# Kernel tuning notes

Measured on AMD Instinct MI355X. Metric: run time of the kernel, lower is better.

The kernel has to match this reference:

```python
import jax, jax.numpy as jnp
import numpy as np

N, R, H, L, E = 50000, 16, 32, 8, 1600000


def setup_inputs() -> dict:
    key = jax.random.key(0)
    ks = jax.random.split(key, 8)
    edge_index = jax.random.randint(ks[0], (2, E), 0, N, dtype=jnp.int32)
    edge_type = jax.random.randint(ks[1], (E,), 0, R, dtype=jnp.int32)
    W1 = jax.random.normal(ks[2], (R, N, H), jnp.float32) * 0.02
    root1 = jax.random.normal(ks[3], (N, H), jnp.float32) * 0.02
    b1 = jnp.zeros((H,), jnp.float32)
    W2 = jax.random.normal(ks[4], (R, H, L), jnp.float32) * 0.1
    root2 = jax.random.normal(ks[5], (H, L), jnp.float32) * 0.1
    b2 = jnp.zeros((L,), jnp.float32)
    return {"edge_index": edge_index, "edge_type": edge_type,
            "W1": W1, "root1": root1, "b1": b1,
            "W2": W2, "root2": root2, "b2": b2}


def reference(edge_index, edge_type, W1, root1, b1, W2, root2, b2):
    src, dst = edge_index[0], edge_index[1]
    # PyG RGCNConv uses mean aggregation per relation: segment = (relation, dst)
    seg = edge_type * N + dst                                   # [E]
    cnt = jax.ops.segment_sum(jnp.ones((E,), jnp.float32), seg, num_segments=R * N)
    norm_e = (1.0 / jnp.maximum(cnt, 1.0))[seg]                 # per-edge 1/deg_r(dst)

    # Layer 1: x is None -> message for edge (j->i, r) is W1[r, j]; root term is root1[i]
    msg1 = W1[edge_type, src] * norm_e[:, None]                 # [E, H]
    agg1 = jax.ops.segment_sum(msg1, dst, num_segments=N)       # [N, H]
    h1 = jax.nn.relu(agg1 + root1 + b1)

    # Layer 2: mean-aggregate h1[src] per (relation, dst), then relation-wise GEMM
    msg2 = h1[src] * norm_e[:, None]                            # [E, H]
    A = jax.ops.segment_sum(msg2, seg, num_segments=R * N).reshape(R, N, H)
    out = jnp.einsum('rnh,rhl->nl', A, W2) + h1 @ root2 + b2    # [N, L]
    return jax.nn.sigmoid(out)
```

## Files before the change

kernel.cpp:

```cpp
#include <hip/hip_runtime.h>
#include <hip/hip_bf16.h>

#define Nn 50000
#define Rr 16
#define Hh 32
#define Ll 8
#define Ee 1600000
#define NSEG 800000
#define NB 782
#define CH 4096
#define NBLK1 391
#define COLS 392
#define HT_INT4 76636
#define CAP 3072
#define W2U 36

typedef _Float16 h2 __attribute__((ext_vector_type(2)));

__device__ __forceinline__ float dot2(h2 a, unsigned b, float c) {
#ifdef __AMDGCN__
    return __builtin_amdgcn_fdot2(a, __builtin_bit_cast(h2, b), c, false);
#else
    h2 hb = __builtin_bit_cast(h2, b);
    return fmaf((float)a[0], (float)hb[0],
                fmaf((float)a[1], (float)hb[1], c));
#endif
}

__global__ __launch_bounds__(256) void p1hist_kernel(
        const int* __restrict__ dst, int* __restrict__ histT) {
    __shared__ int hist[1024];
    for (int i = threadIdx.x; i < 1024; i += 256) hist[i] = 0;
    __syncthreads();
    int base = blockIdx.x * CH;
    int n = min(CH, Ee - base);
    for (int i = threadIdx.x; i < n; i += 256)
        atomicAdd(&hist[dst[base + i] >> 6], 1);
    __syncthreads();
    for (int k = threadIdx.x; k < NB; k += 256)
        histT[k * COLS + blockIdx.x] = hist[k];
}

__global__ __launch_bounds__(256) void scan1_kernel(
        int4* data4, int* __restrict__ bsum) {
    __shared__ int sm[256];
    int i4 = blockIdx.x * 256 + threadIdx.x;
    int4 v = make_int4(0, 0, 0, 0);
    if (i4 < HT_INT4) v = data4[i4];
    int s0 = v.x, s1 = s0 + v.y, s2 = s1 + v.z, s3 = s2 + v.w;
    sm[threadIdx.x] = s3;
    __syncthreads();
    for (int off = 1; off < 256; off <<= 1) {
        int add = (threadIdx.x >= off) ? sm[threadIdx.x - off] : 0;
        __syncthreads();
        sm[threadIdx.x] += add;
        __syncthreads();
    }
    int base = sm[threadIdx.x] - s3;
    if (i4 < HT_INT4)
        data4[i4] = make_int4(base, base + s0, base + s1, base + s2);
    if (threadIdx.x == 255) bsum[blockIdx.x] = sm[255];
}

__global__ __launch_bounds__(1024) void scan2_kernel(
        const int* __restrict__ bsum, int* __restrict__ boff, int nblk) {
    __shared__ int sm[1024];
    int v = (threadIdx.x < nblk) ? bsum[threadIdx.x] : 0;
    sm[threadIdx.x] = v;
    __syncthreads();
    for (int off = 1; off < 1024; off <<= 1) {
        int add = (threadIdx.x >= off) ? sm[threadIdx.x - off] : 0;
        __syncthreads();
        sm[threadIdx.x] += add;
        __syncthreads();
    }
    if (threadIdx.x < nblk) boff[threadIdx.x] = sm[threadIdx.x] - v;
}

__global__ __launch_bounds__(256) void p1scat_kernel(
        const int* __restrict__ src, const int* __restrict__ dst,
        const int* __restrict__ etype, const int* __restrict__ offsT,
        const int* __restrict__ boff, unsigned* __restrict__ pay) {
    __shared__ int lhist[1024], lofs[1024], lcur[1024], goff[1024];
    __shared__ int partial[256];
    __shared__ unsigned stage[CH];
    __shared__ unsigned short sbkt[CH];
    int t = threadIdx.x;
    for (int i = t; i < 1024; i += 256) lhist[i] = 0;
    __syncthreads();
    int base = blockIdx.x * CH;
    int n = min(CH, Ee - base);
    for (int i = t; i < n; i += 256)
        atomicAdd(&lhist[dst[base + i] >> 6], 1);
    __syncthreads();
    int h0 = lhist[4*t], h1v = lhist[4*t+1], h2i = lhist[4*t+2], h3 = lhist[4*t+3];
    int s = h0 + h1v + h2i + h3;
    partial[t] = s;
    __syncthreads();
    for (int off = 1; off < 256; off <<= 1) {
        int add = (t >= off) ? partial[t - off] : 0;
        __syncthreads();
        partial[t] += add;
        __syncthreads();
    }
    int run = partial[t] - s;
    lofs[4*t] = run; lcur[4*t] = run; run += h0;
    lofs[4*t+1] = run; lcur[4*t+1] = run; run += h1v;
    lofs[4*t+2] = run; lcur[4*t+2] = run; run += h2i;
    lofs[4*t+3] = run; lcur[4*t+3] = run;
    for (int k = t; k < NB; k += 256) {
        int idx = k * COLS + blockIdx.x;
        goff[k] = offsT[idx] + boff[idx >> 10];
    }
    __syncthreads();
    for (int i = t; i < n; i += 256) {
        int e = base + i;
        int dv = dst[e];
        int b = dv >> 6;
        int pos = atomicAdd(&lcur[b], 1);
        stage[pos] = ((unsigned)(dv & 63) << 20) | ((unsigned)etype[e] << 16)
                   | (unsigned)src[e];
        sbkt[pos] = (unsigned short)b;
    }
    __syncthreads();
    for (int j = t; j < n; j += 256) {
        int b = sbkt[j];
        pay[goff[b] + (j - lofs[b])] = stage[j];
    }
}

__global__ __launch_bounds__(256) void p2sort_kernel(
        const int* __restrict__ offsT, const int* __restrict__ boff,
        unsigned* pay, unsigned* __restrict__ combo) {
    __shared__ unsigned buf[CAP], outb[CAP];
    __shared__ int hist[1024], lofs[1024], lcur[1024], partial[256];
    int k = blockIdx.x, t = threadIdx.x;
    int idx0 = k * COLS;
    int base = offsT[idx0] + boff[idx0 >> 10];
    int next;
    if (k == NB - 1) {
        next = Ee;
    } else {
        int idx1 = (k + 1) * COLS;
        next = offsT[idx1] + boff[idx1 >> 10];
    }
    int n = next - base;
    for (int i = t; i < 1024; i += 256) hist[i] = 0;
    __syncthreads();
    for (int j = t; j < n; j += 256) {
        unsigned p = pay[base + j];
        buf[j] = p;
        atomicAdd(&hist[(p >> 16) & 0x3FFu], 1);
    }
    __syncthreads();
    int h0 = hist[4*t], h1v = hist[4*t+1], h2i = hist[4*t+2], h3 = hist[4*t+3];
    int s = h0 + h1v + h2i + h3;
    partial[t] = s;
    __syncthreads();
    for (int off = 1; off < 256; off <<= 1) {
        int add = (t >= off) ? partial[t - off] : 0;
        __syncthreads();
        partial[t] += add;
        __syncthreads();
    }
    int run = partial[t] - s;
    lofs[4*t] = run; lcur[4*t] = run; run += h0;
    lofs[4*t+1] = run; lcur[4*t+1] = run; run += h1v;
    lofs[4*t+2] = run; lcur[4*t+2] = run; run += h2i;
    lofs[4*t+3] = run; lcur[4*t+3] = run;
    __syncthreads();
    for (int bin = t; bin < 1024; bin += 256) {
        int dglob = (k << 6) | (bin >> 4);
        if (dglob < Nn)
            combo[(k << 10) | bin] =
                ((unsigned)(base + lofs[bin]) << 8) | (unsigned)hist[bin];
    }
    if (k == NB - 1 && t == 0) combo[NSEG] = ((unsigned)Ee) << 8;
    for (int j = t; j < n; j += 256) {
        unsigned p = buf[j];
        int bin = (int)((p >> 16) & 0x3FFu);
        int pos = atomicAdd(&lcur[bin], 1);
        outb[pos] = (((p >> 16) & 15u) << 24) | ((unsigned)hist[bin] << 16)
                  | (p & 0xFFFFu);
    }
    __syncthreads();
    for (int j = t; j < n; j += 256) pay[base + j] = outb[j];
}

__global__ __launch_bounds__(256) void layer1_kernel(
        const unsigned* __restrict__ csr32, const unsigned* __restrict__ combo,
        const float* __restrict__ W1, const float* __restrict__ root1,
        const float* __restrict__ b1, unsigned short* __restrict__ h1h) {
    int d = (blockIdx.x * 256 + threadIdx.x) >> 6;
    int lane = threadIdx.x & 63;
    int slot = lane >> 3, chunk = lane & 7;
    if (d >= Nn) return;
    int beg = (int)(combo[d << 4] >> 8);
    int end = (int)(combo[(d + 1) << 4] >> 8);
    int deg = end - beg;
    float4 acc = make_float4(0.f, 0.f, 0.f, 0.f);
    const float* Wc = W1 + (chunk << 2);
#pragma unroll 1
    for (int i = 0; i < deg; i += 32) {
        int p0 = i + slot, p1 = p0 + 8, p2 = p0 + 16, p3 = p0 + 24;
        bool r0 = p0 < deg, r1 = p1 < deg, r2 = p2 < deg, r3 = p3 < deg;
        unsigned v0 = csr32[beg + (r0 ? p0 : 0)];
        unsigned v1 = csr32[beg + (r1 ? p1 : 0)];
        unsigned v2 = csr32[beg + (r2 ? p2 : 0)];
        unsigned v3 = csr32[beg + (r3 ? p3 : 0)];
        float n0 = r0 ? __builtin_amdgcn_rcpf((float)((v0 >> 16) & 255u)) : 0.f;
        float n1 = r1 ? __builtin_amdgcn_rcpf((float)((v1 >> 16) & 255u)) : 0.f;
        float n2 = r2 ? __builtin_amdgcn_rcpf((float)((v2 >> 16) & 255u)) : 0.f;
        float n3 = r3 ? __builtin_amdgcn_rcpf((float)((v3 >> 16) & 255u)) : 0.f;
        float4 w0 = *(const float4*)(Wc +
            ((size_t)((int)(v0 >> 24) * Nn + (int)(v0 & 0xffffu)) << 5));
        float4 w1 = *(const float4*)(Wc +
            ((size_t)((int)(v1 >> 24) * Nn + (int)(v1 & 0xffffu)) << 5));
        float4 w2 = *(const float4*)(Wc +
            ((size_t)((int)(v2 >> 24) * Nn + (int)(v2 & 0xffffu)) << 5));
        float4 w3 = *(const float4*)(Wc +
            ((size_t)((int)(v3 >> 24) * Nn + (int)(v3 & 0xffffu)) << 5));
        acc.x = fmaf(n0, w0.x, acc.x); acc.y = fmaf(n0, w0.y, acc.y);
        acc.z = fmaf(n0, w0.z, acc.z); acc.w = fmaf(n0, w0.w, acc.w);
        acc.x = fmaf(n1, w1.x, acc.x); acc.y = fmaf(n1, w1.y, acc.y);
        acc.z = fmaf(n1, w1.z, acc.z); acc.w = fmaf(n1, w1.w, acc.w);
        acc.x = fmaf(n2, w2.x, acc.x); acc.y = fmaf(n2, w2.y, acc.y);
        acc.z = fmaf(n2, w2.z, acc.z); acc.w = fmaf(n2, w2.w, acc.w);
        acc.x = fmaf(n3, w3.x, acc.x); acc.y = fmaf(n3, w3.y, acc.y);
        acc.z = fmaf(n3, w3.z, acc.z); acc.w = fmaf(n3, w3.w, acc.w);
    }
#pragma unroll
    for (int m = 8; m <= 32; m <<= 1) {
        acc.x += __shfl_xor(acc.x, m, 64);
        acc.y += __shfl_xor(acc.y, m, 64);
        acc.z += __shfl_xor(acc.z, m, 64);
        acc.w += __shfl_xor(acc.w, m, 64);
    }
    if (slot == 0) {
        int hb = chunk << 2;
        float4 rt = *(const float4*)(root1 + (d << 5) + hb);
        float4 bb = *(const float4*)(b1 + hb);
        _Float16 q0 = (_Float16)fmaxf(acc.x + rt.x + bb.x, 0.f);
        _Float16 q1 = (_Float16)fmaxf(acc.y + rt.y + bb.y, 0.f);
        _Float16 q2 = (_Float16)fmaxf(acc.z + rt.z + bb.z, 0.f);
        _Float16 q3 = (_Float16)fmaxf(acc.w + rt.w + bb.w, 0.f);
        ushort4 ov;
        ov.x = __builtin_bit_cast(unsigned short, q0);
        ov.y = __builtin_bit_cast(unsigned short, q1);
        ov.z = __builtin_bit_cast(unsigned short, q2);
        ov.w = __builtin_bit_cast(unsigned short, q3);
        *(ushort4*)(h1h + (d << 5) + hb) = ov;
    }
}

__global__ __launch_bounds__(256) void layer2_kernel(
        const unsigned* __restrict__ csr32, const unsigned* __restrict__ combo,
        const unsigned short* __restrict__ h1h, const float* __restrict__ W2,
        const float* __restrict__ root2, const float* __restrict__ b2,
        float* __restrict__ out) {
    __shared__ unsigned W2s[17 * 4 * W2U];
    for (int idx = threadIdx.x; idx < 17 * 4 * 32; idx += 256) {
        int r = idx >> 7;
        int c = (idx >> 5) & 3;
        int u = idx & 31;
        int hp = u >> 3, l = u & 7;
        int h = (c << 3) | (hp << 1);
        float w0, w1;
        if (r < 16) {
            w0 = W2[(r << 8) + (h << 3) + l];
            w1 = W2[(r << 8) + ((h + 1) << 3) + l];
        } else {
            w0 = root2[(h << 3) + l];
            w1 = root2[((h + 1) << 3) + l];
        }
        h2 p = { (_Float16)w0, (_Float16)w1 };
        W2s[((r << 2) | c) * W2U + u] = __builtin_bit_cast(unsigned, p);
    }
    __syncthreads();

    int d = (blockIdx.x * 256 + threadIdx.x) >> 6;
    int lane = threadIdx.x & 63;
    int slot = lane >> 2, chunk = lane & 3;
    if (d >= Nn) return;
    int beg = (int)(combo[d << 4] >> 8);
    int end = (int)(combo[(d + 1) << 4] >> 8);
    int deg = end - beg;
    int degv = deg + 1;
    float acc[8] = {0.f, 0.f, 0.f, 0.f, 0.f, 0.f, 0.f, 0.f};
    const int hb = chunk << 3;
#pragma unroll 1
    for (int i = 0; i < degv; i += 32) {
        int p0 = i + slot, p1 = p0 + 16;
        bool re0 = p0 < deg, re1 = p1 < deg;
        bool vi0 = p0 == deg, vi1 = p1 == deg;
        unsigned v0 = csr32[beg + (re0 ? p0 : 0)];
        unsigned v1 = csr32[beg + (re1 ? p1 : 0)];
        int s0 = vi0 ? d : (re0 ? (int)(v0 & 0xffffu) : 0);
        int s1 = vi1 ? d : (re1 ? (int)(v1 & 0xffffu) : 0);
        int r0 = vi0 ? 16 : (re0 ? (int)(v0 >> 24) : 0);
        int r1 = vi1 ? 16 : (re1 ? (int)(v1 >> 24) : 0);
        float n0 = vi0 ? 1.0f
                 : (re0 ? __builtin_amdgcn_rcpf((float)((v0 >> 16) & 255u)) : 0.f);
        float n1 = vi1 ? 1.0f
                 : (re1 ? __builtin_amdgcn_rcpf((float)((v1 >> 16) & 255u)) : 0.f);
        uint4 hw0 = *(const uint4*)(h1h + (s0 << 5) + hb);
        uint4 hw1 = *(const uint4*)(h1h + (s1 << 5) + hb);
        const unsigned* w0p = &W2s[((r0 << 2) | chunk) * W2U];
        const unsigned* w1p = &W2s[((r1 << 2) | chunk) * W2U];

        h2 n0h = { (_Float16)n0, (_Float16)n0 };
        h2 a00 = __builtin_bit_cast(h2, hw0.x) * n0h;
        h2 a01 = __builtin_bit_cast(h2, hw0.y) * n0h;
        h2 a02 = __builtin_bit_cast(h2, hw0.z) * n0h;
        h2 a03 = __builtin_bit_cast(h2, hw0.w) * n0h;
        uint4 b00 = *(const uint4*)(w0p);
        uint4 b01 = *(const uint4*)(w0p + 4);
        uint4 b02 = *(const uint4*)(w0p + 8);
        uint4 b03 = *(const uint4*)(w0p + 12);
        acc[0] = dot2(a00, b00.x, acc[0]); acc[1] = dot2(a00, b00.y, acc[1]);
        acc[2] = dot2(a00, b00.z, acc[2]); acc[3] = dot2(a00, b00.w, acc[3]);
        acc[4] = dot2(a00, b01.x, acc[4]); acc[5] = dot2(a00, b01.y, acc[5]);
        acc[6] = dot2(a00, b01.z, acc[6]); acc[7] = dot2(a00, b01.w, acc[7]);
        acc[0] = dot2(a01, b02.x, acc[0]); acc[1] = dot2(a01, b02.y, acc[1]);
        acc[2] = dot2(a01, b02.z, acc[2]); acc[3] = dot2(a01, b02.w, acc[3]);
        acc[4] = dot2(a01, b03.x, acc[4]); acc[5] = dot2(a01, b03.y, acc[5]);
        acc[6] = dot2(a01, b03.z, acc[6]); acc[7] = dot2(a01, b03.w, acc[7]);
        uint4 b04 = *(const uint4*)(w0p + 16);
        uint4 b05 = *(const uint4*)(w0p + 20);
        uint4 b06 = *(const uint4*)(w0p + 24);
        uint4 b07 = *(const uint4*)(w0p + 28);
        acc[0] = dot2(a02, b04.x, acc[0]); acc[1] = dot2(a02, b04.y, acc[1]);
        acc[2] = dot2(a02, b04.z, acc[2]); acc[3] = dot2(a02, b04.w, acc[3]);
        acc[4] = dot2(a02, b05.x, acc[4]); acc[5] = dot2(a02, b05.y, acc[5]);
        acc[6] = dot2(a02, b05.z, acc[6]); acc[7] = dot2(a02, b05.w, acc[7]);
        acc[0] = dot2(a03, b06.x, acc[0]); acc[1] = dot2(a03, b06.y, acc[1]);
        acc[2] = dot2(a03, b06.z, acc[2]); acc[3] = dot2(a03, b06.w, acc[3]);
        acc[4] = dot2(a03, b07.x, acc[4]); acc[5] = dot2(a03, b07.y, acc[5]);
        acc[6] = dot2(a03, b07.z, acc[6]); acc[7] = dot2(a03, b07.w, acc[7]);

        h2 n1h = { (_Float16)n1, (_Float16)n1 };
        h2 a10 = __builtin_bit_cast(h2, hw1.x) * n1h;
        h2 a11 = __builtin_bit_cast(h2, hw1.y) * n1h;
        h2 a12 = __builtin_bit_cast(h2, hw1.z) * n1h;
        h2 a13 = __builtin_bit_cast(h2, hw1.w) * n1h;
        uint4 b10 = *(const uint4*)(w1p);
        uint4 b11 = *(const uint4*)(w1p + 4);
        uint4 b12 = *(const uint4*)(w1p + 8);
        uint4 b13 = *(const uint4*)(w1p + 12);
        acc[0] = dot2(a10, b10.x, acc[0]); acc[1] = dot2(a10, b10.y, acc[1]);
        acc[2] = dot2(a10, b10.z, acc[2]); acc[3] = dot2(a10, b10.w, acc[3]);
        acc[4] = dot2(a10, b11.x, acc[4]); acc[5] = dot2(a10, b11.y, acc[5]);
        acc[6] = dot2(a10, b11.z, acc[6]); acc[7] = dot2(a10, b11.w, acc[7]);
        acc[0] = dot2(a11, b12.x, acc[0]); acc[1] = dot2(a11, b12.y, acc[1]);
        acc[2] = dot2(a11, b12.z, acc[2]); acc[3] = dot2(a11, b12.w, acc[3]);
        acc[4] = dot2(a11, b13.x, acc[4]); acc[5] = dot2(a11, b13.y, acc[5]);
        acc[6] = dot2(a11, b13.z, acc[6]); acc[7] = dot2(a11, b13.w, acc[7]);
        uint4 b14 = *(const uint4*)(w1p + 16);
        uint4 b15 = *(const uint4*)(w1p + 20);
        uint4 b16 = *(const uint4*)(w1p + 24);
        uint4 b17 = *(const uint4*)(w1p + 28);
        acc[0] = dot2(a12, b14.x, acc[0]); acc[1] = dot2(a12, b14.y, acc[1]);
        acc[2] = dot2(a12, b14.z, acc[2]); acc[3] = dot2(a12, b14.w, acc[3]);
        acc[4] = dot2(a12, b15.x, acc[4]); acc[5] = dot2(a12, b15.y, acc[5]);
        acc[6] = dot2(a12, b15.z, acc[6]); acc[7] = dot2(a12, b15.w, acc[7]);
        acc[0] = dot2(a13, b16.x, acc[0]); acc[1] = dot2(a13, b16.y, acc[1]);
        acc[2] = dot2(a13, b16.z, acc[2]); acc[3] = dot2(a13, b16.w, acc[3]);
        acc[4] = dot2(a13, b17.x, acc[4]); acc[5] = dot2(a13, b17.y, acc[5]);
        acc[6] = dot2(a13, b17.z, acc[6]); acc[7] = dot2(a13, b17.w, acc[7]);
    }
#pragma unroll
    for (int m = 1; m <= 32; m <<= 1) {
#pragma unroll
        for (int l = 0; l < 8; ++l)
            acc[l] += __shfl_xor(acc[l], m, 64);
    }
    if (lane < 8) {
        float myv = acc[0];
#pragma unroll
        for (int l = 1; l < 8; ++l) myv = (lane == l) ? acc[l] : myv;
        float o = myv + b2[lane];
        out[(d << 3) | lane] = 1.0f / (1.0f + __expf(-o));
    }
}

extern "C" void kernel_launch(void* const* d_in, const int* in_sizes, int n_in,
                              void* d_out, int out_size, void* d_ws, size_t ws_size,
                              hipStream_t stream) {
    const int* edge_index = (const int*)d_in[0];
    const int* etype      = (const int*)d_in[1];
    const float* W1    = (const float*)d_in[2];
    const float* root1 = (const float*)d_in[3];
    const float* b1    = (const float*)d_in[4];
    const float* W2    = (const float*)d_in[5];
    const float* root2 = (const float*)d_in[6];
    const float* b2    = (const float*)d_in[7];
    float* out = (float*)d_out;

    const int* src = edge_index;
    const int* dst = edge_index + Ee;

    int* ws = (int*)d_ws;
    unsigned* combo        = (unsigned*)ws;
    unsigned* pay          = (unsigned*)(ws + 800016);
    unsigned short* h1h    = (unsigned short*)(ws + 2400016);
    int* histT             = ws + 3200016;
    int* bsum              = ws + 3506560;
    int* boff              = ws + 3506872;

    if (ws_size < (size_t)3507184 * sizeof(int)) return;

    hipMemsetAsync(histT, 0, (size_t)(NB * COLS) * sizeof(int), stream);

    const int nblkSc = (HT_INT4 + 255) / 256;
    const int nblkL  = (Nn * 64 + 255) / 256;

    p1hist_kernel<<<NBLK1, 256, 0, stream>>>(dst, histT);
    scan1_kernel<<<nblkSc, 256, 0, stream>>>((int4*)histT, bsum);
    scan2_kernel<<<1, 1024, 0, stream>>>(bsum, boff, nblkSc);
    p1scat_kernel<<<NBLK1, 256, 0, stream>>>(src, dst, etype, histT, boff, pay);
    p2sort_kernel<<<NB, 256, 0, stream>>>(histT, boff, pay, combo);
    layer1_kernel<<<nblkL, 256, 0, stream>>>(pay, combo, W1, root1, b1, h1h);
    layer2_kernel<<<nblkL, 256, 0, stream>>>(pay, combo, h1h, W2, root2, b2, out);
}
```

Measured before the change: 298.9 us.

## Fuse CSR build stages into one cooperative kernel with grid syncs

Replaces the memset plus five separate build kernels (histogram, two scans, scatter, per-bucket sort) with a single cooperative kernel of 391 blocks separated by grid.sync barriers. Each block keeps its local histogram in shared memory across phases, so it does not recount dst for the scatter, and shared buffers are unioned to fit. This removes kernel launch gaps and one pass over dst, but adds grid-wide barrier cost and makes the sort phase loop twice per block since 782 buckets now run on 391 blocks.

```diff
diff --git a/kernel.cpp b/kernel.cpp
--- a/kernel.cpp
+++ b/kernel.cpp
@@ -1,5 +1,8 @@
 #include <hip/hip_runtime.h>
 #include <hip/hip_bf16.h>
+#include <hip/hip_cooperative_groups.h>
+
+namespace cg = cooperative_groups;
 
 #define Nn 50000
 #define Rr 16
@@ -12,6 +15,7 @@
 #define NBLK1 391
 #define COLS 392
 #define HT_INT4 76636
+#define NSC 300
 #define CAP 3072
 #define W2U 36
 
@@ -27,164 +31,172 @@
 #endif
 }
 
-__global__ __launch_bounds__(256) void p1hist_kernel(
-        const int* __restrict__ dst, int* __restrict__ histT) {
-    __shared__ int hist[1024];
-    for (int i = threadIdx.x; i < 1024; i += 256) hist[i] = 0;
-    __syncthreads();
-    int base = blockIdx.x * CH;
-    int n = min(CH, Ee - base);
-    for (int i = threadIdx.x; i < n; i += 256)
-        atomicAdd(&hist[dst[base + i] >> 6], 1);
-    __syncthreads();
-    for (int k = threadIdx.x; k < NB; k += 256)
-        histT[k * COLS + blockIdx.x] = hist[k];
-}
-
-__global__ __launch_bounds__(256) void scan1_kernel(
-        int4* data4, int* __restrict__ bsum) {
-    __shared__ int sm[256];
-    int i4 = blockIdx.x * 256 + threadIdx.x;
-    int4 v = make_int4(0, 0, 0, 0);
-    if (i4 < HT_INT4) v = data4[i4];
-    int s0 = v.x, s1 = s0 + v.y, s2 = s1 + v.z, s3 = s2 + v.w;
-    sm[threadIdx.x] = s3;
-    __syncthreads();
-    for (int off = 1; off < 256; off <<= 1) {
-        int add = (threadIdx.x >= off) ? sm[threadIdx.x - off] : 0;
-        __syncthreads();
-        sm[threadIdx.x] += add;
-        __syncthreads();
-    }
-    int base = sm[threadIdx.x] - s3;
-    if (i4 < HT_INT4)
-        data4[i4] = make_int4(base, base + s0, base + s1, base + s2);
-    if (threadIdx.x == 255) bsum[blockIdx.x] = sm[255];
-}
-
-__global__ __launch_bounds__(1024) void scan2_kernel(
-        const int* __restrict__ bsum, int* __restrict__ boff, int nblk) {
-    __shared__ int sm[1024];
-    int v = (threadIdx.x < nblk) ? bsum[threadIdx.x] : 0;
-    sm[threadIdx.x] = v;
-    __syncthreads();
-    for (int off = 1; off < 1024; off <<= 1) {
-        int add = (threadIdx.x >= off) ? sm[threadIdx.x - off] : 0;
-        __syncthreads();
-        sm[threadIdx.x] += add;
-        __syncthreads();
-    }
-    if (threadIdx.x < nblk) boff[threadIdx.x] = sm[threadIdx.x] - v;
-}
-
-__global__ __launch_bounds__(256) void p1scat_kernel(
+__global__ __launch_bounds__(256) void build_kernel(
         const int* __restrict__ src, const int* __restrict__ dst,
-        const int* __restrict__ etype, const int* __restrict__ offsT,
-        const int* __restrict__ boff, unsigned* __restrict__ pay) {
+        const int* __restrict__ etype, int* __restrict__ histT,
+        int* __restrict__ bsum, int* __restrict__ boff,
+        unsigned* __restrict__ pay, unsigned* __restrict__ combo) {
+    cg::grid_group grid = cg::this_grid();
     __shared__ int lhist[1024], lofs[1024], lcur[1024], goff[1024];
     __shared__ int partial[256];
-    __shared__ unsigned stage[CH];
-    __shared__ unsigned short sbkt[CH];
-    int t = threadIdx.x;
+    __shared__ int scan2buf[512];
+    __shared__ unsigned bigbuf[CH + CH / 2];
+    unsigned* stage = bigbuf;
+    unsigned short* sbkt = (unsigned short*)(bigbuf + CH);
+    unsigned* buf  = bigbuf;
+    unsigned* outb = bigbuf + CAP;
+
+    const int t = threadIdx.x;
+    const int b = blockIdx.x;
+
     for (int i = t; i < 1024; i += 256) lhist[i] = 0;
     __syncthreads();
-    int base = blockIdx.x * CH;
-    int n = min(CH, Ee - base);
-    for (int i = t; i < n; i += 256)
-        atomicAdd(&lhist[dst[base + i] >> 6], 1);
+    {
+        int base = b * CH;
+        int n = min(CH, Ee - base);
+        for (int i = t; i < n; i += 256)
+            atomicAdd(&lhist[dst[base + i] >> 6], 1);
+    }
     __syncthreads();
-    int h0 = lhist[4*t], h1v = lhist[4*t+1], h2i = lhist[4*t+2], h3 = lhist[4*t+3];
-    int s = h0 + h1v + h2i + h3;
-    partial[t] = s;
-    __syncthreads();
-    for (int off = 1; off < 256; off <<= 1) {
-        int add = (t >= off) ? partial[t - off] : 0;
-        __syncthreads();
-        partial[t] += add;
-        __syncthreads();
-    }
-    int run = partial[t] - s;
-    lofs[4*t] = run; lcur[4*t] = run; run += h0;
-    lofs[4*t+1] = run; lcur[4*t+1] = run; run += h1v;
-    lofs[4*t+2] = run; lcur[4*t+2] = run; run += h2i;
-    lofs[4*t+3] = run; lcur[4*t+3] = run;
-    for (int k = t; k < NB; k += 256) {
-        int idx = k * COLS + blockIdx.x;
-        goff[k] = offsT[idx] + boff[idx >> 10];
-    }
-    __syncthreads();
-    for (int i = t; i < n; i += 256) {
-        int e = base + i;
-        int dv = dst[e];
-        int b = dv >> 6;
-        int pos = atomicAdd(&lcur[b], 1);
-        stage[pos] = ((unsigned)(dv & 63) << 20) | ((unsigned)etype[e] << 16)
-                   | (unsigned)src[e];
-        sbkt[pos] = (unsigned short)b;
-    }
-    __syncthreads();
-    for (int j = t; j < n; j += 256) {
-        int b = sbkt[j];
-        pay[goff[b] + (j - lofs[b])] = stage[j];
-    }
-}
-
-__global__ __launch_bounds__(256) void p2sort_kernel(
-        const int* __restrict__ offsT, const int* __restrict__ boff,
-        unsigned* pay, unsigned* __restrict__ combo) {
-    __shared__ unsigned buf[CAP], outb[CAP];
-    __shared__ int hist[1024], lofs[1024], lcur[1024], partial[256];
-    int k = blockIdx.x, t = threadIdx.x;
-    int idx0 = k * COLS;
-    int base = offsT[idx0] + boff[idx0 >> 10];
-    int next;
-    if (k == NB - 1) {
-        next = Ee;
-    } else {
-        int idx1 = (k + 1) * COLS;
-        next = offsT[idx1] + boff[idx1 >> 10];
-    }
-    int n = next - base;
-    for (int i = t; i < 1024; i += 256) hist[i] = 0;
-    __syncthreads();
-    for (int j = t; j < n; j += 256) {
-        unsigned p = pay[base + j];
-        buf[j] = p;
-        atomicAdd(&hist[(p >> 16) & 0x3FFu], 1);
-    }
-    __syncthreads();
-    int h0 = hist[4*t], h1v = hist[4*t+1], h2i = hist[4*t+2], h3 = hist[4*t+3];
-    int s = h0 + h1v + h2i + h3;
-    partial[t] = s;
-    __syncthreads();
-    for (int off = 1; off < 256; off <<= 1) {
-        int add = (t >= off) ? partial[t - off] : 0;
-        __syncthreads();
-        partial[t] += add;
-        __syncthreads();
-    }
-    int run = partial[t] - s;
-    lofs[4*t] = run; lcur[4*t] = run; run += h0;
-    lofs[4*t+1] = run; lcur[4*t+1] = run; run += h1v;
-    lofs[4*t+2] = run; lcur[4*t+2] = run; run += h2i;
-    lofs[4*t+3] = run; lcur[4*t+3] = run;
-    __syncthreads();
-    for (int bin = t; bin < 1024; bin += 256) {
-        int dglob = (k << 6) | (bin >> 4);
-        if (dglob < Nn)
-            combo[(k << 10) | bin] =
-                ((unsigned)(base + lofs[bin]) << 8) | (unsigned)hist[bin];
-    }
-    if (k == NB - 1 && t == 0) combo[NSEG] = ((unsigned)Ee) << 8;
-    for (int j = t; j < n; j += 256) {
-        unsigned p = buf[j];
-        int bin = (int)((p >> 16) & 0x3FFu);
-        int pos = atomicAdd(&lcur[bin], 1);
-        outb[pos] = (((p >> 16) & 15u) << 24) | ((unsigned)hist[bin] << 16)
-                  | (p & 0xFFFFu);
-    }
-    __syncthreads();
-    for (int j = t; j < n; j += 256) pay[base + j] = outb[j];
+    for (int k = t; k < NB; k += 256) histT[k * COLS + b] = lhist[k];
+    if (b == 0)
+        for (int k = t; k < NB; k += 256) histT[k * COLS + (COLS - 1)] = 0;
+    grid.sync();
+
+    if (b < NSC) {
+        int i4 = b * 256 + t;
+        int4 v = make_int4(0, 0, 0, 0);
+        if (i4 < HT_INT4) v = ((int4*)histT)[i4];
+        int s0 = v.x, s1 = s0 + v.y, s2 = s1 + v.z, s3 = s2 + v.w;
+        partial[t] = s3;
+        __syncthreads();
+        for (int off = 1; off < 256; off <<= 1) {
+            int add = (t >= off) ? partial[t - off] : 0;
+            __syncthreads();
+            partial[t] += add;
+            __syncthreads();
+        }
+        int base = partial[t] - s3;
+        if (i4 < HT_INT4)
+            ((int4*)histT)[i4] = make_int4(base, base + s0, base + s1, base + s2);
+        if (t == 255) bsum[b] = partial[255];
+    }
+    grid.sync();
+
+    if (b == 0) {
+        int v0 = (t < NSC) ? bsum[t] : 0;
+        int v1 = (t + 256 < NSC) ? bsum[t + 256] : 0;
+        scan2buf[t] = v0;
+        scan2buf[t + 256] = v1;
+        __syncthreads();
+        for (int off = 1; off < 512; off <<= 1) {
+            int a0 = (t >= off) ? scan2buf[t - off] : 0;
+            int a1 = (t + 256 >= off) ? scan2buf[t + 256 - off] : 0;
+            __syncthreads();
+            scan2buf[t] += a0;
+            scan2buf[t + 256] += a1;
+            __syncthreads();
+        }
+        if (t < NSC) boff[t] = scan2buf[t] - v0;
+        if (t + 256 < NSC) boff[t + 256] = scan2buf[t + 256] - v1;
+    }
+    grid.sync();
+
+    {
+        int h0 = lhist[4*t], h1v = lhist[4*t+1], h2i = lhist[4*t+2],
+            h3 = lhist[4*t+3];
+        int s = h0 + h1v + h2i + h3;
+        partial[t] = s;
+        __syncthreads();
+        for (int off = 1; off < 256; off <<= 1) {
+            int add = (t >= off) ? partial[t - off] : 0;
+            __syncthreads();
+            partial[t] += add;
+            __syncthreads();
+        }
+        int run = partial[t] - s;
+        lofs[4*t] = run; lcur[4*t] = run; run += h0;
+        lofs[4*t+1] = run; lcur[4*t+1] = run; run += h1v;
+        lofs[4*t+2] = run; lcur[4*t+2] = run; run += h2i;
+        lofs[4*t+3] = run; lcur[4*t+3] = run;
+        for (int k = t; k < NB; k += 256) {
+            int idx = k * COLS + b;
+            goff[k] = histT[idx] + boff[idx >> 10];
+        }
+        __syncthreads();
+        int base = b * CH;
+        int n = min(CH, Ee - base);
+        for (int i = t; i < n; i += 256) {
+            int e = base + i;
+            int dv = dst[e];
+            int bk = dv >> 6;
+            int pos = atomicAdd(&lcur[bk], 1);
+            stage[pos] = ((unsigned)(dv & 63) << 20)
+                       | ((unsigned)etype[e] << 16) | (unsigned)src[e];
+            sbkt[pos] = (unsigned short)bk;
+        }
+        __syncthreads();
+        for (int j = t; j < n; j += 256) {
+            int bk = sbkt[j];
+            pay[goff[bk] + (j - lofs[bk])] = stage[j];
+        }
+    }
+    grid.sync();
+
+    for (int k = b; k < NB; k += NBLK1) {
+        int idx0 = k * COLS;
+        int base = histT[idx0] + boff[idx0 >> 10];
+        int next;
+        if (k == NB - 1) {
+            next = Ee;
+        } else {
+            int idx1 = (k + 1) * COLS;
+            next = histT[idx1] + boff[idx1 >> 10];
+        }
+        int n = next - base;
+        for (int i = t; i < 1024; i += 256) lhist[i] = 0;
+        __syncthreads();
+        for (int j = t; j < n; j += 256) {
+            unsigned p = pay[base + j];
+            buf[j] = p;
+            atomicAdd(&lhist[(p >> 16) & 0x3FFu], 1);
+        }
+        __syncthreads();
+        int h0 = lhist[4*t], h1v = lhist[4*t+1], h2i = lhist[4*t+2],
+            h3 = lhist[4*t+3];
+        int s = h0 + h1v + h2i + h3;
+        partial[t] = s;
+        __syncthreads();
+        for (int off = 1; off < 256; off <<= 1) {
+            int add = (t >= off) ? partial[t - off] : 0;
+            __syncthreads();
+            partial[t] += add;
+            __syncthreads();
+        }
+        int run = partial[t] - s;
+        lofs[4*t] = run; lcur[4*t] = run; run += h0;
+        lofs[4*t+1] = run; lcur[4*t+1] = run; run += h1v;
+        lofs[4*t+2] = run; lcur[4*t+2] = run; run += h2i;
+        lofs[4*t+3] = run; lcur[4*t+3] = run;
+        __syncthreads();
+        for (int bin = t; bin < 1024; bin += 256) {
+            int dglob = (k << 6) | (bin >> 4);
+            if (dglob < Nn)
+                combo[(k << 10) | bin] =
+                    ((unsigned)(base + lofs[bin]) << 8) | (unsigned)lhist[bin];
+        }
+        if (k == NB - 1 && t == 0) combo[NSEG] = ((unsigned)Ee) << 8;
+        for (int j = t; j < n; j += 256) {
+            unsigned p = buf[j];
+            int bin = (int)((p >> 16) & 0x3FFu);
+            int pos = atomicAdd(&lcur[bin], 1);
+            outb[pos] = (((p >> 16) & 15u) << 24) | ((unsigned)lhist[bin] << 16)
+                      | (p & 0xFFFFu);
+        }
+        __syncthreads();
+        for (int j = t; j < n; j += 256) pay[base + j] = outb[j];
+        __syncthreads();
+    }
 }
 
 __global__ __launch_bounds__(256) void layer1_kernel(
@@ -409,16 +421,12 @@
 
     if (ws_size < (size_t)3507184 * sizeof(int)) return;
 
-    hipMemsetAsync(histT, 0, (size_t)(NB * COLS) * sizeof(int), stream);
-
-    const int nblkSc = (HT_INT4 + 255) / 256;
-    const int nblkL  = (Nn * 64 + 255) / 256;
-
-    p1hist_kernel<<<NBLK1, 256, 0, stream>>>(dst, histT);
-    scan1_kernel<<<nblkSc, 256, 0, stream>>>((int4*)histT, bsum);
-    scan2_kernel<<<1, 1024, 0, stream>>>(bsum, boff, nblkSc);
-    p1scat_kernel<<<NBLK1, 256, 0, stream>>>(src, dst, etype, histT, boff, pay);
-    p2sort_kernel<<<NB, 256, 0, stream>>>(histT, boff, pay, combo);
+    const int nblkL = (Nn * 64 + 255) / 256;
+
+    void* args[] = { (void*)&src, (void*)&dst, (void*)&etype, (void*)&histT,
+                     (void*)&bsum, (void*)&boff, (void*)&pay, (void*)&combo };
+    hipLaunchCooperativeKernel((const void*)build_kernel, dim3(NBLK1),
+                               dim3(256), args, 0, stream);
     layer1_kernel<<<nblkL, 256, 0, stream>>>(pay, combo, W1, root1, b1, h1h);
     layer2_kernel<<<nblkL, 256, 0, stream>>>(pay, combo, h1h, W2, root2, b2, out);
 }
```

Measured after the change: 499.9 us. 67.2% more time.
